# Performance work log

Hardware: AMD Instinct MI355X
Metric: run time of the kernel (lower is better)

## Reference

```python
import jax, jax.numpy as jnp
import numpy as np

N_NODES = 100000
N_EDGES = 1200000
N_GRAPHS = 128
D_IN = 64
D_HID = 64
N_CLASSES = 10


def gcn_conv(x, row, col, W, b):
    """PyG GCNConv: h = x@W; add self-loops; sym-norm deg^-1/2 gather-scatter; + bias."""
    n = x.shape[0]
    h = x @ W  # [N, out]
    loop = jnp.arange(n)
    r = jnp.concatenate([row, loop])
    c = jnp.concatenate([col, loop])
    deg = jax.ops.segment_sum(jnp.ones_like(c, dtype=x.dtype), c, num_segments=n)
    dinv = jax.lax.rsqrt(jnp.maximum(deg, 1.0))  # with self-loops deg >= 1
    norm = dinv[r] * dinv[c]  # [E+N]
    msg = h[r] * norm[:, None]  # gather + per-edge scale
    out = jax.ops.segment_sum(msg, c, num_segments=n)  # scatter-add at targets
    return out + b


def global_mean_pool(x, batch, num_graphs):
    s = jax.ops.segment_sum(x, batch, num_segments=num_graphs)
    cnt = jax.ops.segment_sum(jnp.ones((x.shape[0],), dtype=x.dtype), batch, num_segments=num_graphs)
    return s / jnp.maximum(cnt, 1.0)[:, None]


def setup_inputs() -> dict:
    key = jax.random.key(0)
    ks = jax.random.split(key, 12)
    x = jax.random.normal(ks[0], (N_NODES, D_IN), dtype=jnp.float32)
    edge_index = jax.random.randint(ks[1], (2, N_EDGES), 0, N_NODES, dtype=jnp.int64)
    batch = jnp.sort(jax.random.randint(ks[2], (N_NODES,), 0, N_GRAPHS, dtype=jnp.int64))

    def glorot(k, fan_in, fan_out):
        lim = (6.0 / (fan_in + fan_out)) ** 0.5
        return jax.random.uniform(k, (fan_in, fan_out), jnp.float32, -lim, lim)

    return {
        "x": x,
        "edge_index": edge_index,
        "batch": batch,
        "W1": glorot(ks[3], D_IN, D_HID),
        "b1": jnp.zeros((D_HID,), jnp.float32),
        "W2": glorot(ks[4], D_HID, D_HID),
        "b2": jnp.zeros((D_HID,), jnp.float32),
        "W3": glorot(ks[5], D_HID, D_HID),
        "b3": jnp.zeros((D_HID,), jnp.float32),
        "linW": glorot(ks[6], D_HID, N_CLASSES),
        "linb": jnp.zeros((N_CLASSES,), jnp.float32),
    }


def reference(x, edge_index, batch, W1, b1, W2, b2, W3, b3, linW, linb):
    row, col = edge_index[0], edge_index[1]
    h = jax.nn.relu(gcn_conv(x, row, col, W1, b1))
    h = jax.nn.relu(gcn_conv(h, row, col, W2, b2))
    h = gcn_conv(h, row, col, W3, b3)
    g = global_mean_pool(h, batch, N_GRAPHS)  # [B, hidden]
    # dropout p=0.5 is identity in eval mode (training=False)
    return g @ linW + linb  # [B, num_classes]
```

## Files before the change

kernel.cpp:

```cpp
#include <hip/hip_runtime.h>
#include <hip/hip_bf16.h>


#define N_NODES 100000
#define N_EDGES 1200000
#define N_GRAPHS 128
#define D 64
#define N_CLASSES 10

#define NB 512
#define BSZ 196
#define PEB 4096
#define PEB4 (PEB/4)

typedef unsigned short ushort_t;

__device__ __forceinline__ float bf2f(ushort_t u) {
    union { unsigned int i; float f; } v;
    v.i = ((unsigned int)u) << 16;
    return v.f;
}
__device__ __forceinline__ ushort_t f2bf(float f) {
    __hip_bfloat16 hb = __float2bfloat16(f);
    return *(ushort_t*)&hb;
}

__global__ void init_k(int* __restrict__ bcount,
                       float* __restrict__ gsum, float* __restrict__ cnt) {
    int i = blockIdx.x * 256 + threadIdx.x;
    if (i < NB) bcount[i] = 0;
    if (i < N_GRAPHS * D) gsum[i] = 0.0f;
    if (i < N_GRAPHS) cnt[i] = 0.0f;
}

__global__ void count_k(const int4* __restrict__ col4, int* __restrict__ bcount,
                        const int* __restrict__ batch, float* __restrict__ cnt,
                        int E4, int n) {
    __shared__ int h[NB];
    __shared__ int bh[N_GRAPHS];
    for (int i = threadIdx.x; i < NB; i += 256) h[i] = 0;
    if (threadIdx.x < N_GRAPHS) bh[threadIdx.x] = 0;
    __syncthreads();
    int base = blockIdx.x * PEB4;
#pragma unroll
    for (int k = 0; k < 4; ++k) {
        int idx = base + k * 256 + threadIdx.x;
        if (idx < E4) {
            int4 c = col4[idx];
            atomicAdd(&h[c.x / BSZ], 1);
            atomicAdd(&h[c.y / BSZ], 1);
            atomicAdd(&h[c.z / BSZ], 1);
            atomicAdd(&h[c.w / BSZ], 1);
        }
    }
    for (int i = blockIdx.x * 256 + threadIdx.x; i < n; i += gridDim.x * 256)
        atomicAdd(&bh[batch[i]], 1);
    __syncthreads();
    for (int i = threadIdx.x; i < NB; i += 256)
        if (h[i]) atomicAdd(&bcount[i], h[i]);
    if (threadIdx.x < N_GRAPHS && bh[threadIdx.x])
        atomicAdd(&cnt[threadIdx.x], (float)bh[threadIdx.x]);
}

__global__ void scan_k(const int* __restrict__ bcount, int* __restrict__ bstart,
                       int* __restrict__ bcursor) {
    __shared__ int s[NB];
    int t = threadIdx.x;
    int v0 = bcount[t];
    s[t] = v0;
    __syncthreads();
    for (int off = 1; off < NB; off <<= 1) {
        int v = (t >= off) ? s[t - off] : 0;
        __syncthreads();
        s[t] += v;
        __syncthreads();
    }
    int ex = s[t] - v0;
    bstart[t] = ex;
    bcursor[t] = ex;
}

__global__ void scatter_k(const int4* __restrict__ row4, const int4* __restrict__ col4,
                          int* __restrict__ bcursor, int* __restrict__ part, int E4) {
    __shared__ int h[NB], gb[NB], c2[NB];
    for (int i = threadIdx.x; i < NB; i += 256) { h[i] = 0; c2[i] = 0; }
    __syncthreads();
    int base = blockIdx.x * PEB4;
    int4 rr[4], cc[4];
    bool ok[4];
#pragma unroll
    for (int k = 0; k < 4; ++k) {
        int idx = base + k * 256 + threadIdx.x;
        ok[k] = idx < E4;
        if (ok[k]) {
            rr[k] = row4[idx];
            cc[k] = col4[idx];
            atomicAdd(&h[cc[k].x / BSZ], 1);
            atomicAdd(&h[cc[k].y / BSZ], 1);
            atomicAdd(&h[cc[k].z / BSZ], 1);
            atomicAdd(&h[cc[k].w / BSZ], 1);
        }
    }
    __syncthreads();
    for (int i = threadIdx.x; i < NB; i += 256)
        if (h[i]) gb[i] = atomicAdd(&bcursor[i], h[i]);
    __syncthreads();
#pragma unroll
    for (int k = 0; k < 4; ++k) {
        if (ok[k]) {
            int r[4] = { rr[k].x, rr[k].y, rr[k].z, rr[k].w };
            int c[4] = { cc[k].x, cc[k].y, cc[k].z, cc[k].w };
#pragma unroll
            for (int j = 0; j < 4; ++j) {
                int bk = c[j] / BSZ;
                int dl = c[j] - bk * BSZ;
                int rk = atomicAdd(&c2[bk], 1);
                part[gb[bk] + rk] = (r[j] << 8) | dl;
            }
        }
    }
}

__global__ void sortbuild_k(const int* __restrict__ part, const int* __restrict__ bstart,
                            const int* __restrict__ bcount, int* __restrict__ csr,
                            int* __restrict__ deg, int* __restrict__ cursor,
                            float* __restrict__ dinv) {
    __shared__ int h[256], st[256], c2[256];
    int b = blockIdx.x, t = threadIdx.x;
    int ebeg = bstart[b];
    int cntE = bcount[b];
    h[t] = 0; c2[t] = 0;
    __syncthreads();
    for (int e = ebeg + t; e < ebeg + cntE; e += 256)
        atomicAdd(&h[part[e] & 255], 1);
    __syncthreads();
    int hv = h[t];
    for (int off = 1; off < 256; off <<= 1) {
        int v = (t >= off) ? h[t - off] : 0;
        __syncthreads();
        h[t] += v;
        __syncthreads();
    }
    st[t] = h[t] - hv;
    __syncthreads();
    int node = b * BSZ + t;
    if (t < BSZ && node < N_NODES) {
        deg[node] = hv;
        dinv[node] = rsqrtf((float)(hv + 1));
        cursor[node] = ebeg + st[t] + hv;
    }
    for (int e = ebeg + t; e < ebeg + cntE; e += 256) {
        int p = part[e];
        int cl = p & 255;
        int rk = atomicAdd(&c2[cl], 1);
        csr[ebeg + st[cl] + rk] = p >> 8;
    }
}

__global__ __launch_bounds__(256) void gemm_f32_k(
        const float* __restrict__ X, const float* __restrict__ W,
        const float* __restrict__ dinv, ushort_t* __restrict__ H, int n) {
    __shared__ float Xs[4][D];
    int tid = threadIdx.x, wave = tid >> 6, lane = tid & 63;
    float wcol[D];
#pragma unroll
    for (int k = 0; k < D; ++k) wcol[k] = W[k * D + lane];
    for (int row0 = blockIdx.x * 4; row0 < n; row0 += gridDim.x * 4) {
        int row = row0 + wave;
        if (row < n) {
            Xs[wave][lane] = X[(size_t)row * D + lane];
            float acc = 0.0f;
#pragma unroll
            for (int k = 0; k < D; ++k) acc += Xs[wave][k] * wcol[k];
            H[(size_t)row * D + lane] = f2bf(acc * dinv[row]);
        }
    }
}

__global__ __launch_bounds__(256) void gemm_bf16_k(
        const ushort_t* __restrict__ U, const float* __restrict__ W,
        const float* __restrict__ dinv, ushort_t* __restrict__ H, int n) {
    __shared__ float Xs[4][D];
    int tid = threadIdx.x, wave = tid >> 6, lane = tid & 63;
    float wcol[D];
#pragma unroll
    for (int k = 0; k < D; ++k) wcol[k] = W[k * D + lane];
    for (int row0 = blockIdx.x * 4; row0 < n; row0 += gridDim.x * 4) {
        int row = row0 + wave;
        if (row < n) {
            Xs[wave][lane] = fmaxf(bf2f(U[(size_t)row * D + lane]), 0.0f);
            float acc = 0.0f;
#pragma unroll
            for (int k = 0; k < D; ++k) acc += Xs[wave][k] * wcol[k];
            H[(size_t)row * D + lane] = f2bf(acc * dinv[row]);
        }
    }
}

__global__ void gather_k(const ushort_t* __restrict__ Hp, const int* __restrict__ csr,
                         const int* __restrict__ cursor, const int* __restrict__ deg,
                         const float* __restrict__ dinv, const float* __restrict__ b,
                         ushort_t* __restrict__ O, int n) {
    int c = blockIdx.x * 4 + (threadIdx.x >> 6);
    if (c >= n) return;
    int lane = threadIdx.x & 63;
    int end = cursor[c];
    int dg = deg[c];
    float acc = bf2f(Hp[(size_t)c * D + lane]);
    for (int j = end - dg; j < end; j += 64) {
        int idx = j + lane;
        int s = (idx < end) ? csr[idx] : 0;
        int cnt = min(64, end - j);
        int k = 0;
        for (; k + 4 <= cnt; k += 4) {
            int r0 = __shfl(s, k);
            int r1 = __shfl(s, k + 1);
            int r2 = __shfl(s, k + 2);
            int r3 = __shfl(s, k + 3);
            float v0 = bf2f(Hp[(size_t)r0 * D + lane]);
            float v1 = bf2f(Hp[(size_t)r1 * D + lane]);
            float v2 = bf2f(Hp[(size_t)r2 * D + lane]);
            float v3 = bf2f(Hp[(size_t)r3 * D + lane]);
            acc += v0 + v1 + v2 + v3;
        }
        for (; k < cnt; ++k) {
            int r0 = __shfl(s, k);
            acc += bf2f(Hp[(size_t)r0 * D + lane]);
        }
    }
    O[(size_t)c * D + lane] = f2bf(b[lane] + dinv[c] * acc);
}

__global__ void gather_pool_k(const ushort_t* __restrict__ Hp, const int* __restrict__ csr,
                              const int* __restrict__ cursor, const int* __restrict__ deg,
                              const float* __restrict__ dinv, const float* __restrict__ b,
                              const int* __restrict__ batch, float* __restrict__ gsum,
                              int n) {
    int c = blockIdx.x * 4 + (threadIdx.x >> 6);
    if (c >= n) return;
    int lane = threadIdx.x & 63;
    int end = cursor[c];
    int dg = deg[c];
    float acc = bf2f(Hp[(size_t)c * D + lane]);
    for (int j = end - dg; j < end; j += 64) {
        int idx = j + lane;
        int s = (idx < end) ? csr[idx] : 0;
        int cnt = min(64, end - j);
        int k = 0;
        for (; k + 4 <= cnt; k += 4) {
            int r0 = __shfl(s, k);
            int r1 = __shfl(s, k + 1);
            int r2 = __shfl(s, k + 2);
            int r3 = __shfl(s, k + 3);
            float v0 = bf2f(Hp[(size_t)r0 * D + lane]);
            float v1 = bf2f(Hp[(size_t)r1 * D + lane]);
            float v2 = bf2f(Hp[(size_t)r2 * D + lane]);
            float v3 = bf2f(Hp[(size_t)r3 * D + lane]);
            acc += v0 + v1 + v2 + v3;
        }
        for (; k < cnt; ++k) {
            int r0 = __shfl(s, k);
            acc += bf2f(Hp[(size_t)r0 * D + lane]);
        }
    }
    float val = b[lane] + dinv[c] * acc;
    atomicAdd(&gsum[batch[c] * D + lane], val);
}

__global__ void final_k(const float* __restrict__ gsum, const float* __restrict__ cnt,
                        const float* __restrict__ linW, const float* __restrict__ linb,
                        float* __restrict__ out) {
    int tid = blockIdx.x * 256 + threadIdx.x;
    if (tid >= N_GRAPHS * N_CLASSES) return;
    int b = tid / N_CLASSES, c = tid % N_CLASSES;
    float inv = 1.0f / fmaxf(cnt[b], 1.0f);
    float acc = linb[c];
#pragma unroll
    for (int k = 0; k < D; ++k)
        acc += gsum[b * D + k] * inv * linW[k * N_CLASSES + c];
    out[tid] = acc;
}

extern "C" void kernel_launch(void* const* d_in, const int* in_sizes, int n_in,
                              void* d_out, int out_size, void* d_ws, size_t ws_size,
                              hipStream_t stream) {
    const float* x    = (const float*)d_in[0];
    const int*   ei   = (const int*)  d_in[1];
    const int*   batch= (const int*)  d_in[2];
    const float* W1   = (const float*)d_in[3];
    const float* b1   = (const float*)d_in[4];
    const float* W2   = (const float*)d_in[5];
    const float* b2   = (const float*)d_in[6];
    const float* W3   = (const float*)d_in[7];
    const float* b3   = (const float*)d_in[8];
    const float* linW = (const float*)d_in[9];
    const float* linb = (const float*)d_in[10];
    float* out = (float*)d_out;

    const int N = N_NODES, E = N_EDGES, E4 = N_EDGES / 4;
    const int4* row4 = (const int4*)ei;
    const int4* col4 = (const int4*)(ei + E);

    int* wsi = (int*)d_ws;
    float* dinv   = (float*)wsi;
    int*   deg    = wsi + 100352;
    int*   cursor = deg + 100352;
    int*   csr    = cursor + 100352;
    int*   part   = csr + 1200128;
    int*   bcount = part + 1200128;
    int*   bstart = bcount + 512;
    int*   bcursor= bstart + 512;
    ushort_t* bufH = (ushort_t*)(bcursor + 512);
    ushort_t* bufA = bufH + (size_t)N * D;
    float* gsum   = (float*)(bufA + (size_t)N * D);
    float* cnt    = gsum + N_GRAPHS * D;

    const int nb_part  = (E + PEB - 1) / PEB;
    const int nb_gather= (N + 3) / 4;
    const int nb_gemm  = 2048;

    init_k<<<(N_GRAPHS * D + 255) / 256, 256, 0, stream>>>(bcount, gsum, cnt);
    count_k<<<nb_part, 256, 0, stream>>>(col4, bcount, batch, cnt, E4, N);
    scan_k<<<1, NB, 0, stream>>>(bcount, bstart, bcursor);
    scatter_k<<<nb_part, 256, 0, stream>>>(row4, col4, bcursor, part, E4);
    sortbuild_k<<<NB, 256, 0, stream>>>(part, bstart, bcount, csr, deg, cursor, dinv);

    gemm_f32_k<<<nb_gemm, 256, 0, stream>>>(x, W1, dinv, bufH, N);
    gather_k<<<nb_gather, 256, 0, stream>>>(bufH, csr, cursor, deg, dinv, b1, bufA, N);
    gemm_bf16_k<<<nb_gemm, 256, 0, stream>>>(bufA, W2, dinv, bufH, N);
    gather_k<<<nb_gather, 256, 0, stream>>>(bufH, csr, cursor, deg, dinv, b2, bufA, N);
    gemm_bf16_k<<<nb_gemm, 256, 0, stream>>>(bufA, W3, dinv, bufH, N);
    gather_pool_k<<<nb_gather, 256, 0, stream>>>(bufH, csr, cursor, deg, dinv, b3,
                                                 batch, gsum, N);

    final_k<<<(N_GRAPHS * N_CLASSES + 255) / 256, 256, 0, stream>>>(gsum, cnt, linW, linb, out);
}
```

Baseline: 397.6 us.

## Gather two edges per wave with packed bf16 pairs, split pooling, shuffle-based GEMV

The gather kernel now reads 32-bit packed bf16 pairs, so each half-wave handles a different source edge and two neighbors are processed per load instruction. The halves are combined with a cross-lane shuffle before the self-term, bias and scale are applied. The last layer's gather no longer issues one atomic per node into the pooled sums. It writes bf16 output, and a separate pool kernel reduces runs of same-graph nodes before issuing atomics. The per-row GEMM replaces the LDS staging with wave shuffles and uses two accumulators, at the cost of an extra kernel launch and an extra pass over the hidden features.

Result: slower. 503.0 us (+26.5%).

```diff
diff --git a/kernel.cpp b/kernel.cpp
--- a/kernel.cpp
+++ b/kernel.cpp
@@ -14,6 +14,7 @@
 #define PEB4 (PEB/4)
 
 typedef unsigned short ushort_t;
+typedef unsigned int uint_t;
 
 __device__ __forceinline__ float bf2f(ushort_t u) {
     union { unsigned int i; float f; } v;
@@ -160,7 +161,6 @@
 __global__ __launch_bounds__(256) void gemm_f32_k(
         const float* __restrict__ X, const float* __restrict__ W,
         const float* __restrict__ dinv, ushort_t* __restrict__ H, int n) {
-    __shared__ float Xs[4][D];
     int tid = threadIdx.x, wave = tid >> 6, lane = tid & 63;
     float wcol[D];
 #pragma unroll
@@ -168,11 +168,14 @@
     for (int row0 = blockIdx.x * 4; row0 < n; row0 += gridDim.x * 4) {
         int row = row0 + wave;
         if (row < n) {
-            Xs[wave][lane] = X[(size_t)row * D + lane];
-            float acc = 0.0f;
-#pragma unroll
-            for (int k = 0; k < D; ++k) acc += Xs[wave][k] * wcol[k];
-            H[(size_t)row * D + lane] = f2bf(acc * dinv[row]);
+            float xv = X[(size_t)row * D + lane];
+            float a0 = 0.0f, a1 = 0.0f;
+#pragma unroll
+            for (int k = 0; k < D; k += 2) {
+                a0 += __shfl(xv, k) * wcol[k];
+                a1 += __shfl(xv, k + 1) * wcol[k + 1];
+            }
+            H[(size_t)row * D + lane] = f2bf((a0 + a1) * dinv[row]);
         }
     }
 }
@@ -180,7 +183,6 @@
 __global__ __launch_bounds__(256) void gemm_bf16_k(
         const ushort_t* __restrict__ U, const float* __restrict__ W,
         const float* __restrict__ dinv, ushort_t* __restrict__ H, int n) {
-    __shared__ float Xs[4][D];
     int tid = threadIdx.x, wave = tid >> 6, lane = tid & 63;
     float wcol[D];
 #pragma unroll
@@ -188,83 +190,98 @@
     for (int row0 = blockIdx.x * 4; row0 < n; row0 += gridDim.x * 4) {
         int row = row0 + wave;
         if (row < n) {
-            Xs[wave][lane] = fmaxf(bf2f(U[(size_t)row * D + lane]), 0.0f);
-            float acc = 0.0f;
-#pragma unroll
-            for (int k = 0; k < D; ++k) acc += Xs[wave][k] * wcol[k];
-            H[(size_t)row * D + lane] = f2bf(acc * dinv[row]);
-        }
-    }
-}
-
-__global__ void gather_k(const ushort_t* __restrict__ Hp, const int* __restrict__ csr,
-                         const int* __restrict__ cursor, const int* __restrict__ deg,
-                         const float* __restrict__ dinv, const float* __restrict__ b,
-                         ushort_t* __restrict__ O, int n) {
+            float xv = fmaxf(bf2f(U[(size_t)row * D + lane]), 0.0f);
+            float a0 = 0.0f, a1 = 0.0f;
+#pragma unroll
+            for (int k = 0; k < D; k += 2) {
+                a0 += __shfl(xv, k) * wcol[k];
+                a1 += __shfl(xv, k + 1) * wcol[k + 1];
+            }
+            H[(size_t)row * D + lane] = f2bf((a0 + a1) * dinv[row]);
+        }
+    }
+}
+
+__global__ void gather2_k(const uint_t* __restrict__ Hp2, const int* __restrict__ csr,
+                          const int* __restrict__ cursor, const int* __restrict__ deg,
+                          const float* __restrict__ dinv, const float* __restrict__ b,
+                          uint_t* __restrict__ O2, int n) {
     int c = blockIdx.x * 4 + (threadIdx.x >> 6);
     if (c >= n) return;
     int lane = threadIdx.x & 63;
+    int half = lane >> 5;
+    int col = lane & 31;
     int end = cursor[c];
     int dg = deg[c];
-    float acc = bf2f(Hp[(size_t)c * D + lane]);
+    float ax = 0.0f, ay = 0.0f;
     for (int j = end - dg; j < end; j += 64) {
         int idx = j + lane;
         int s = (idx < end) ? csr[idx] : 0;
-        int cnt = min(64, end - j);
+        int m = min(64, end - j);
         int k = 0;
-        for (; k + 4 <= cnt; k += 4) {
-            int r0 = __shfl(s, k);
-            int r1 = __shfl(s, k + 1);
-            int r2 = __shfl(s, k + 2);
-            int r3 = __shfl(s, k + 3);
-            float v0 = bf2f(Hp[(size_t)r0 * D + lane]);
-            float v1 = bf2f(Hp[(size_t)r1 * D + lane]);
-            float v2 = bf2f(Hp[(size_t)r2 * D + lane]);
-            float v3 = bf2f(Hp[(size_t)r3 * D + lane]);
-            acc += v0 + v1 + v2 + v3;
-        }
-        for (; k < cnt; ++k) {
-            int r0 = __shfl(s, k);
-            acc += bf2f(Hp[(size_t)r0 * D + lane]);
-        }
-    }
-    O[(size_t)c * D + lane] = f2bf(b[lane] + dinv[c] * acc);
-}
-
-__global__ void gather_pool_k(const ushort_t* __restrict__ Hp, const int* __restrict__ csr,
-                              const int* __restrict__ cursor, const int* __restrict__ deg,
-                              const float* __restrict__ dinv, const float* __restrict__ b,
-                              const int* __restrict__ batch, float* __restrict__ gsum,
-                              int n) {
-    int c = blockIdx.x * 4 + (threadIdx.x >> 6);
-    if (c >= n) return;
+        for (; k + 8 <= m; k += 8) {
+#pragma unroll
+            for (int p = 0; p < 4; ++p) {
+                int eA = __shfl(s, k + 2 * p);
+                int eB = __shfl(s, k + 2 * p + 1);
+                int src = half ? eB : eA;
+                uint_t u = Hp2[(size_t)src * 32 + col];
+                ax += bf2f((ushort_t)(u & 0xffff));
+                ay += bf2f((ushort_t)(u >> 16));
+            }
+        }
+        for (; k + 2 <= m; k += 2) {
+            int eA = __shfl(s, k);
+            int eB = __shfl(s, k + 1);
+            int src = half ? eB : eA;
+            uint_t u = Hp2[(size_t)src * 32 + col];
+            ax += bf2f((ushort_t)(u & 0xffff));
+            ay += bf2f((ushort_t)(u >> 16));
+        }
+        if (k < m) {
+            int eA = __shfl(s, k);
+            if (!half) {
+                uint_t u = Hp2[(size_t)eA * 32 + col];
+                ax += bf2f((ushort_t)(u & 0xffff));
+                ay += bf2f((ushort_t)(u >> 16));
+            }
+        }
+    }
+    float bx = __shfl(ax, lane ^ 32);
+    float by = __shfl(ay, lane ^ 32);
+    ax += bx; ay += by;
+    if (half == 0) {
+        uint_t su = Hp2[(size_t)c * 32 + col];
+        ax += bf2f((ushort_t)(su & 0xffff));
+        ay += bf2f((ushort_t)(su >> 16));
+        float2 bb = ((const float2*)b)[col];
+        float di = dinv[c];
+        uint_t lo = f2bf(bb.x + di * ax);
+        uint_t hi = f2bf(bb.y + di * ay);
+        O2[(size_t)c * 32 + col] = lo | (hi << 16);
+    }
+}
+
+#define POOL_CHUNK 64
+__global__ void pool_k(const ushort_t* __restrict__ H, const int* __restrict__ batch,
+                       float* __restrict__ gsum, int n) {
+    int wid = blockIdx.x * 4 + (threadIdx.x >> 6);
     int lane = threadIdx.x & 63;
-    int end = cursor[c];
-    int dg = deg[c];
-    float acc = bf2f(Hp[(size_t)c * D + lane]);
-    for (int j = end - dg; j < end; j += 64) {
-        int idx = j + lane;
-        int s = (idx < end) ? csr[idx] : 0;
-        int cnt = min(64, end - j);
-        int k = 0;
-        for (; k + 4 <= cnt; k += 4) {
-            int r0 = __shfl(s, k);
-            int r1 = __shfl(s, k + 1);
-            int r2 = __shfl(s, k + 2);
-            int r3 = __shfl(s, k + 3);
-            float v0 = bf2f(Hp[(size_t)r0 * D + lane]);
-            float v1 = bf2f(Hp[(size_t)r1 * D + lane]);
-            float v2 = bf2f(Hp[(size_t)r2 * D + lane]);
-            float v3 = bf2f(Hp[(size_t)r3 * D + lane]);
-            acc += v0 + v1 + v2 + v3;
-        }
-        for (; k < cnt; ++k) {
-            int r0 = __shfl(s, k);
-            acc += bf2f(Hp[(size_t)r0 * D + lane]);
-        }
-    }
-    float val = b[lane] + dinv[c] * acc;
-    atomicAdd(&gsum[batch[c] * D + lane], val);
+    int start = wid * POOL_CHUNK;
+    if (start >= n) return;
+    int m = min(POOL_CHUNK, n - start);
+    int bv = batch[min(start + lane, n - 1)];
+    int cur = __shfl(bv, 0);
+    float acc = 0.0f;
+    for (int k = 0; k < m; ++k) {
+        int bb = __shfl(bv, k);
+        if (bb != cur) {
+            atomicAdd(&gsum[cur * D + lane], acc);
+            cur = bb; acc = 0.0f;
+        }
+        acc += bf2f(H[(size_t)(start + k) * D + lane]);
+    }
+    atomicAdd(&gsum[cur * D + lane], acc);
 }
 
 __global__ void final_k(const float* __restrict__ gsum, const float* __restrict__ cnt,
@@ -318,6 +335,8 @@
     const int nb_part  = (E + PEB - 1) / PEB;
     const int nb_gather= (N + 3) / 4;
     const int nb_gemm  = 2048;
+    const int nwaves   = (N + POOL_CHUNK - 1) / POOL_CHUNK;
+    const int nb_pool  = (nwaves + 3) / 4;
 
     init_k<<<(N_GRAPHS * D + 255) / 256, 256, 0, stream>>>(bcount, gsum, cnt);
     count_k<<<nb_part, 256, 0, stream>>>(col4, bcount, batch, cnt, E4, N);
@@ -326,12 +345,15 @@
     sortbuild_k<<<NB, 256, 0, stream>>>(part, bstart, bcount, csr, deg, cursor, dinv);
 
     gemm_f32_k<<<nb_gemm, 256, 0, stream>>>(x, W1, dinv, bufH, N);
-    gather_k<<<nb_gather, 256, 0, stream>>>(bufH, csr, cursor, deg, dinv, b1, bufA, N);
+    gather2_k<<<nb_gather, 256, 0, stream>>>((uint_t*)bufH, csr, cursor, deg, dinv, b1,
+                                             (uint_t*)bufA, N);
     gemm_bf16_k<<<nb_gemm, 256, 0, stream>>>(bufA, W2, dinv, bufH, N);
-    gather_k<<<nb_gather, 256, 0, stream>>>(bufH, csr, cursor, deg, dinv, b2, bufA, N);
+    gather2_k<<<nb_gather, 256, 0, stream>>>((uint_t*)bufH, csr, cursor, deg, dinv, b2,
+                                             (uint_t*)bufA, N);
     gemm_bf16_k<<<nb_gemm, 256, 0, stream>>>(bufA, W3, dinv, bufH, N);
-    gather_pool_k<<<nb_gather, 256, 0, stream>>>(bufH, csr, cursor, deg, dinv, b3,
-                                                 batch, gsum, N);
-
+    gather2_k<<<nb_gather, 256, 0, stream>>>((uint_t*)bufH, csr, cursor, deg, dinv, b3,
+                                             (uint_t*)bufA, N);
+
+    pool_k<<<nb_pool, 256, 0, stream>>>(bufA, batch, gsum, N);
     final_k<<<(N_GRAPHS * N_CLASSES + 255) / 256, 256, 0, stream>>>(gsum, cnt, linW, linb, out);
 }
```
